# Kernel optimization log

Measured on AMD Instinct MI355X. Metric: run time of the kernel, lower is better.

Reference implementation:

```python
import jax, jax.numpy as jnp
import numpy as np

B, C, N = 8, 256, 2048
H = max(1, C // 8)  # hidden = in_channels // 8 = 32


def setup_inputs() -> dict:
    key = jax.random.key(0)
    ks = jax.random.split(key, 7)
    s = 0.05
    return {
        "x": jax.random.normal(ks[0], (B, C, N), dtype=jnp.float32),
        "wq": jax.random.normal(ks[1], (H, C), dtype=jnp.float32) * s,
        "bq": jax.random.normal(ks[2], (H,), dtype=jnp.float32) * s,
        "wk": jax.random.normal(ks[3], (H, C), dtype=jnp.float32) * s,
        "bk": jax.random.normal(ks[4], (H,), dtype=jnp.float32) * s,
        "wv": jax.random.normal(ks[5], (C, C), dtype=jnp.float32) * s,
        "bv": jax.random.normal(ks[6], (C,), dtype=jnp.float32) * s,
    }


def reference(x, wq, bq, wk, bk, wv, bv):
    # 1x1 Conv1d == per-position linear: weight [out, in]
    q = jnp.einsum('bcn,hc->bnh', x, wq) + bq                  # [B, N, H] (already permuted)
    k = jnp.einsum('bcn,hc->bhn', x, wk) + bk[None, :, None]   # [B, H, N]
    v = jnp.einsum('bcn,dc->bdn', x, wv) + bv[None, :, None]   # [B, C, N]
    energy = jnp.einsum('bnh,bhm->bnm', q, k)                  # [B, N, N] (no scaling, as in source)
    weights = jax.nn.softmax(energy, axis=-1)                  # softmax over last dim
    # out = bmm(value, weights^T): out[b,c,i] = sum_j v[b,c,j] * weights[b,i,j]
    out = jnp.einsum('bcj,bij->bci', v, weights)               # [B, C, N]
    return out + x
```

## Files before the change

kernel.cpp:

```cpp
#include <hip/hip_runtime.h>
#include <hip/hip_bf16.h>
#include <cstdint>
#include <cstddef>

#define B_ 8
#define C_ 256
#define N_ 2048
#define H_ 32
#define VP_ 2064
#define NT_ (N_ / 64)

typedef __bf16 bf8 __attribute__((ext_vector_type(8)));
typedef __bf16 bf4 __attribute__((ext_vector_type(4)));
typedef float f4 __attribute__((ext_vector_type(4)));
typedef float f16v __attribute__((ext_vector_type(16)));

__device__ inline void gload_lds16(const void* g, void* l) {
  __builtin_amdgcn_global_load_lds(
      (const __attribute__((address_space(1))) unsigned int*)g,
      (__attribute__((address_space(3))) unsigned int*)l, 16, 0, 0);
}

__global__ __launch_bounds__(256) void pack_kernel(
    const float* __restrict__ wq, const float* __restrict__ wk,
    const float* __restrict__ wv, const float* __restrict__ bq,
    const float* __restrict__ bk, const float* __restrict__ bv,
    __hip_bfloat16* __restrict__ wpk, float* __restrict__ bpk) {
  const float L2E = 1.44269504088896f;
  int r = blockIdx.x, c = threadIdx.x;
  float v;
  if (r < 256)      v = wv[r * 256 + c];
  else if (r < 288) v = wq[(r - 256) * 256 + c] * L2E;
  else              v = wk[(r - 288) * 256 + c];
  wpk[r * 256 + c] = __float2bfloat16(v);
  if (c == 0) bpk[r] = (r < 256) ? bv[r] : (r < 288 ? bq[r - 256] * L2E : bk[r - 288]);
}

__global__ __launch_bounds__(256) void proj_kernel(
    const float* __restrict__ x, const __hip_bfloat16* __restrict__ wpk,
    const float* __restrict__ bpk, __hip_bfloat16* __restrict__ vbf,
    __hip_bfloat16* __restrict__ qkb) {
  __shared__ __attribute__((aligned(16))) __hip_bfloat16 As[2][320 * 32];
  int tid = threadIdx.x, wv = tid >> 6, lane = tid & 63;
  int b = blockIdx.y;
  int n0 = blockIdx.x * 32;
  int fcol = lane & 15, hi4 = lane >> 4;
  int grow = lane >> 2, gc = (lane & 3) * 8;
  const float* xb = x + (size_t)b * C_ * N_;

#pragma unroll
  for (int g = 0; g < 5; ++g)
    gload_lds16(wpk + (size_t)(wv * 80 + g * 16 + grow) * 256 + gc,
                &As[0][(wv * 80 + g * 16) * 32]);
  float xr[2][8];
#pragma unroll
  for (int j = 0; j < 2; ++j)
#pragma unroll
    for (int e = 0; e < 8; ++e)
      xr[j][e] = xb[(size_t)(hi4 * 8 + e) * N_ + n0 + j * 16 + fcol];

  f4 acc[5][2] = {};
  for (int t = 0; t < 8; ++t) {
    int buf = t & 1;
    __syncthreads();
    if (t < 7) {
      int k1 = (t + 1) * 32;
#pragma unroll
      for (int g = 0; g < 5; ++g)
        gload_lds16(wpk + (size_t)(wv * 80 + g * 16 + grow) * 256 + k1 + gc,
                    &As[buf ^ 1][(wv * 80 + g * 16) * 32]);
    }
    bf8 bfr[2];
#pragma unroll
    for (int j = 0; j < 2; ++j)
#pragma unroll
      for (int e = 0; e < 8; ++e) bfr[j][e] = (__bf16)xr[j][e];
    if (t < 7) {
      int k1 = (t + 1) * 32;
#pragma unroll
      for (int j = 0; j < 2; ++j)
#pragma unroll
        for (int e = 0; e < 8; ++e)
          xr[j][e] = xb[(size_t)(k1 + hi4 * 8 + e) * N_ + n0 + j * 16 + fcol];
    }
#pragma unroll
    for (int s = 0; s < 5; ++s) {
      bf8 af = *(const bf8*)&As[buf][(wv * 80 + s * 16 + fcol) * 32 + hi4 * 8];
      acc[s][0] = __builtin_amdgcn_mfma_f32_16x16x32_bf16(af, bfr[0], acc[s][0], 0, 0, 0);
      acc[s][1] = __builtin_amdgcn_mfma_f32_16x16x32_bf16(af, bfr[1], acc[s][1], 0, 0, 0);
    }
  }
  int rq = hi4 * 4;
#pragma unroll
  for (int s = 0; s < 5; ++s)
#pragma unroll
    for (int r = 0; r < 4; ++r) {
      int m = wv * 80 + s * 16 + rq + r;
      float bias = bpk[m];
#pragma unroll
      for (int j = 0; j < 2; ++j) {
        int n = n0 + j * 16 + fcol;
        float val = acc[s][j][r] + bias;
        if (m < 256)
          vbf[((size_t)b * C_ + m) * VP_ + n] = __float2bfloat16(val);
        else
          qkb[((size_t)b * N_ + n) * 64 + (m - 256)] = __float2bfloat16(val);
      }
    }
}

#define ATTN_BODY(T, BUF, KC0, KC1, KN0, KN1, VC0, VC1, VC2, VC3)              \
  {                                                                            \
    const __hip_bfloat16* pr_ = &pS[BUF][l31][hi * 8];                         \
    bf8 pf0_ = *(const bf8*)(pr_ + 0);                                         \
    bf8 pf4_ = *(const bf8*)(pr_ + 32 * 88);                                   \
    bf8 pf1_ = *(const bf8*)(pr_ + 16);                                        \
    bf8 pf5_ = *(const bf8*)(pr_ + 32 * 88 + 16);                              \
    bf8 pf2_ = *(const bf8*)(pr_ + 32);                                        \
    bf8 pf6_ = *(const bf8*)(pr_ + 32 * 88 + 32);                              \
    bf8 pf3_ = *(const bf8*)(pr_ + 48);                                        \
    bf8 pf7_ = *(const bf8*)(pr_ + 32 * 88 + 48);                              \
    f16v s_ = {};                                                              \
    if ((T) + 1 < NT_) {                                                       \
      s_ = __builtin_amdgcn_mfma_f32_32x32x16_bf16(KC0, qf0, s_, 0, 0, 0);     \
      s_ = __builtin_amdgcn_mfma_f32_32x32x16_bf16(KC1, qf1, s_, 0, 0, 0);     \
    }                                                                          \
    {                                                                          \
      int tn_ = (T) + 2 < NT_ ? (T) + 2 : NT_ - 1;                             \
      const __hip_bfloat16* kpn_ = kp + (size_t)tn_ * 64 * 64;                 \
      KN0 = *(const bf8*)kpn_;                                                 \
      KN1 = *(const bf8*)(kpn_ + 16);                                          \
    }                                                                          \
    __builtin_amdgcn_s_setprio(1);                                             \
    acc0 = __builtin_amdgcn_mfma_f32_32x32x16_bf16(VC0, pf0_, acc0, 0, 0, 0);  \
    acc1 = __builtin_amdgcn_mfma_f32_32x32x16_bf16(VC0, pf4_, acc1, 0, 0, 0);  \
    acc0 = __builtin_amdgcn_mfma_f32_32x32x16_bf16(VC1, pf1_, acc0, 0, 0, 0);  \
    acc1 = __builtin_amdgcn_mfma_f32_32x32x16_bf16(VC1, pf5_, acc1, 0, 0, 0);  \
    acc0 = __builtin_amdgcn_mfma_f32_32x32x16_bf16(VC2, pf2_, acc0, 0, 0, 0);  \
    acc1 = __builtin_amdgcn_mfma_f32_32x32x16_bf16(VC2, pf6_, acc1, 0, 0, 0);  \
    acc0 = __builtin_amdgcn_mfma_f32_32x32x16_bf16(VC3, pf3_, acc0, 0, 0, 0);  \
    acc1 = __builtin_amdgcn_mfma_f32_32x32x16_bf16(VC3, pf7_, acc1, 0, 0, 0);  \
    __builtin_amdgcn_s_setprio(0);                                             \
    {                                                                          \
      int tn_ = (T) + 2 < NT_ ? (T) + 2 : NT_ - 1;                             \
      const __hip_bfloat16* vpn_ = vR + tn_ * 64;                              \
      VC0 = *(const bf8*)vpn_;                                                 \
      VC1 = *(const bf8*)(vpn_ + 16);                                          \
      VC2 = *(const bf8*)(vpn_ + 32);                                          \
      VC3 = *(const bf8*)(vpn_ + 48);                                          \
    }                                                                          \
    if ((T) + 1 < NT_) {                                                       \
      _Pragma("unroll")                                                        \
      for (int r = 0; r < 16; ++r) s_[r] = __builtin_amdgcn_exp2f(s_[r]);      \
      _Pragma("unroll")                                                        \
      for (int r = 0; r < 16; r += 2) { lp0 += s_[r]; lp1 += s_[r + 1]; }      \
      __hip_bfloat16* pw_ = &pS[(BUF) ^ 1][ws_i * 32 + l31][ws_j * 32 + 4 * hi];\
      _Pragma("unroll")                                                        \
      for (int q = 0; q < 4; ++q) {                                            \
        bf4 tb_;                                                               \
        tb_[0] = (__bf16)s_[4 * q + 0];                                        \
        tb_[1] = (__bf16)s_[4 * q + 1];                                        \
        tb_[2] = (__bf16)s_[4 * q + 2];                                        \
        tb_[3] = (__bf16)s_[4 * q + 3];                                        \
        *(bf4*)(pw_ + 8 * q) = tb_;                                            \
      }                                                                        \
      asm volatile("s_waitcnt lgkmcnt(0)" ::: "memory");                       \
      __builtin_amdgcn_sched_barrier(0);                                       \
      __builtin_amdgcn_s_barrier();                                            \
      __builtin_amdgcn_sched_barrier(0);                                       \
    }                                                                          \
  }

__global__ __launch_bounds__(256, 2) void fused_attn(
    const __hip_bfloat16* __restrict__ qk,
    const __hip_bfloat16* __restrict__ vbf,
    const float* __restrict__ x, float* __restrict__ out) {
  __shared__ __attribute__((aligned(16))) __hip_bfloat16 pS[2][64][88];
  __shared__ float lSp[2][64];
  int tid = threadIdx.x;
  int wv = tid >> 6, lane = tid & 63;
  int l31 = lane & 31, hi = lane >> 5;
  int ws_i = wv >> 1, ws_j = wv & 1;
  int blk = blockIdx.x;
  int b = blk & 7;
  int rest = blk >> 3;
  int c0 = (rest & 1) * 128;
  int i0 = (rest >> 1) * 64;

  const __hip_bfloat16* qkB = qk + (size_t)b * N_ * 64;
  const __hip_bfloat16* qp = qkB + (size_t)(i0 + ws_i * 32 + l31) * 64 + hi * 8;
  bf8 qf0 = *(const bf8*)qp;
  bf8 qf1 = *(const bf8*)(qp + 16);
  const __hip_bfloat16* kp = qkB + (size_t)(ws_j * 32 + l31) * 64 + 32 + hi * 8;
  const __hip_bfloat16* vR =
      vbf + ((size_t)b * C_ + c0 + wv * 32 + l31) * VP_ + hi * 8;

  bf8 k00 = *(const bf8*)kp;
  bf8 k01 = *(const bf8*)(kp + 16);
  bf8 kO0 = *(const bf8*)(kp + 64 * 64);
  bf8 kO1 = *(const bf8*)(kp + 64 * 64 + 16);
  bf8 kE0, kE1;
  bf8 vE0 = *(const bf8*)vR;
  bf8 vE1 = *(const bf8*)(vR + 16);
  bf8 vE2 = *(const bf8*)(vR + 32);
  bf8 vE3 = *(const bf8*)(vR + 48);
  bf8 vO0 = *(const bf8*)(vR + 64);
  bf8 vO1 = *(const bf8*)(vR + 64 + 16);
  bf8 vO2 = *(const bf8*)(vR + 64 + 32);
  bf8 vO3 = *(const bf8*)(vR + 64 + 48);

  f16v acc0 = {}, acc1 = {};
  float lp0 = 0.f, lp1 = 0.f;

  {
    f16v s_ = {};
    s_ = __builtin_amdgcn_mfma_f32_32x32x16_bf16(k00, qf0, s_, 0, 0, 0);
    s_ = __builtin_amdgcn_mfma_f32_32x32x16_bf16(k01, qf1, s_, 0, 0, 0);
#pragma unroll
    for (int r = 0; r < 16; ++r) s_[r] = __builtin_amdgcn_exp2f(s_[r]);
#pragma unroll
    for (int r = 0; r < 16; r += 2) { lp0 += s_[r]; lp1 += s_[r + 1]; }
    __hip_bfloat16* pw_ = &pS[0][ws_i * 32 + l31][ws_j * 32 + 4 * hi];
#pragma unroll
    for (int q = 0; q < 4; ++q) {
      bf4 tb_;
      tb_[0] = (__bf16)s_[4 * q + 0];
      tb_[1] = (__bf16)s_[4 * q + 1];
      tb_[2] = (__bf16)s_[4 * q + 2];
      tb_[3] = (__bf16)s_[4 * q + 3];
      *(bf4*)(pw_ + 8 * q) = tb_;
    }
    asm volatile("s_waitcnt lgkmcnt(0)" ::: "memory");
    __builtin_amdgcn_sched_barrier(0);
    __builtin_amdgcn_s_barrier();
    __builtin_amdgcn_sched_barrier(0);
  }

  for (int tt = 0; tt < NT_; tt += 2) {
    ATTN_BODY(tt,     0, kO0, kO1, kE0, kE1, vE0, vE1, vE2, vE3)
    ATTN_BODY(tt + 1, 1, kE0, kE1, kO0, kO1, vO0, vO1, vO2, vO3)
  }
#undef ATTN_BODY

  float lp = lp0 + lp1;
  lp += __shfl_xor(lp, 32);
  if (lane < 32) lSp[ws_j][ws_i * 32 + l31] = lp;
  __syncthreads();
  float linv0 = 1.0f / (lSp[0][l31] + lSp[1][l31]);
  float linv1 = 1.0f / (lSp[0][32 + l31] + lSp[1][32 + l31]);

  const float* xr = x + (size_t)b * C_ * N_;
  float* op = out + (size_t)b * C_ * N_;
#pragma unroll
  for (int r = 0; r < 16; ++r) {
    int crow = (r & 3) + 8 * (r >> 2) + 4 * hi;
    size_t o = (size_t)(c0 + wv * 32 + crow) * N_ + i0 + l31;
    op[o] = acc0[r] * linv0 + xr[o];
    op[o + 32] = acc1[r] * linv1 + xr[o + 32];
  }
}

extern "C" void kernel_launch(void* const* d_in, const int* in_sizes, int n_in,
                              void* d_out, int out_size, void* d_ws, size_t ws_size,
                              hipStream_t stream) {
  const float* x  = (const float*)d_in[0];
  const float* wq = (const float*)d_in[1];
  const float* bq = (const float*)d_in[2];
  const float* wk = (const float*)d_in[3];
  const float* bk = (const float*)d_in[4];
  const float* wv = (const float*)d_in[5];
  const float* bv = (const float*)d_in[6];
  float* out = (float*)d_out;

  char* ws = (char*)d_ws;
  __hip_bfloat16* qkb = (__hip_bfloat16*)ws;
  __hip_bfloat16* vbf = (__hip_bfloat16*)(ws + (2u << 20));
  __hip_bfloat16* wpk = (__hip_bfloat16*)(ws + 10551296u);
  float*          bpk = (float*)(ws + 10551296u + 163840u);

  pack_kernel<<<dim3(320), 256, 0, stream>>>(wq, wk, wv, bq, bk, bv, wpk, bpk);
  proj_kernel<<<dim3(N_ / 32, B_), 256, 0, stream>>>(x, wpk, bpk, vbf, qkb);
  fused_attn<<<dim3(512), 256, 0, stream>>>(qkb, vbf, x, out);
}
```

Measured before the change: 128.2 us.

## Switch attention MFMAs from 32x32x16 to 16x16x32 bf16 tiles

```diff
diff --git a/kernel.cpp b/kernel.cpp
--- a/kernel.cpp
+++ b/kernel.cpp
@@ -13,7 +13,6 @@
 typedef __bf16 bf8 __attribute__((ext_vector_type(8)));
 typedef __bf16 bf4 __attribute__((ext_vector_type(4)));
 typedef float f4 __attribute__((ext_vector_type(4)));
-typedef float f16v __attribute__((ext_vector_type(16)));
 
 __device__ inline void gload_lds16(const void* g, void* l) {
   __builtin_amdgcn_global_load_lds(
@@ -109,60 +108,81 @@
     }
 }
 
-#define ATTN_BODY(T, BUF, KC0, KC1, KN0, KN1, VC0, VC1, VC2, VC3)              \
+#define MFMA16(A, B, C) __builtin_amdgcn_mfma_f32_16x16x32_bf16(A, B, C, 0, 0, 0)
+
+#define ATTN_BODY(T, BUF, KC0, KC1, KN0, KN1, VA, VB, VC, VD)                  \
   {                                                                            \
-    const __hip_bfloat16* pr_ = &pS[BUF][l31][hi * 8];                         \
-    bf8 pf0_ = *(const bf8*)(pr_ + 0);                                         \
-    bf8 pf4_ = *(const bf8*)(pr_ + 32 * 88);                                   \
-    bf8 pf1_ = *(const bf8*)(pr_ + 16);                                        \
-    bf8 pf5_ = *(const bf8*)(pr_ + 32 * 88 + 16);                              \
-    bf8 pf2_ = *(const bf8*)(pr_ + 32);                                        \
-    bf8 pf6_ = *(const bf8*)(pr_ + 32 * 88 + 32);                              \
-    bf8 pf3_ = *(const bf8*)(pr_ + 48);                                        \
-    bf8 pf7_ = *(const bf8*)(pr_ + 32 * 88 + 48);                              \
-    f16v s_ = {};                                                              \
+    bf8 pf00 = *(const bf8*)&pS[BUF][ 0 + li][ 0 + lg8];                       \
+    bf8 pf10 = *(const bf8*)&pS[BUF][16 + li][ 0 + lg8];                       \
+    bf8 pf20 = *(const bf8*)&pS[BUF][32 + li][ 0 + lg8];                       \
+    bf8 pf30 = *(const bf8*)&pS[BUF][48 + li][ 0 + lg8];                       \
+    bf8 pf01 = *(const bf8*)&pS[BUF][ 0 + li][32 + lg8];                       \
+    bf8 pf11 = *(const bf8*)&pS[BUF][16 + li][32 + lg8];                       \
+    bf8 pf21 = *(const bf8*)&pS[BUF][32 + li][32 + lg8];                       \
+    bf8 pf31 = *(const bf8*)&pS[BUF][48 + li][32 + lg8];                       \
+    f4 s00 = {}, s01 = {}, s10 = {}, s11 = {};                                 \
     if ((T) + 1 < NT_) {                                                       \
-      s_ = __builtin_amdgcn_mfma_f32_32x32x16_bf16(KC0, qf0, s_, 0, 0, 0);     \
-      s_ = __builtin_amdgcn_mfma_f32_32x32x16_bf16(KC1, qf1, s_, 0, 0, 0);     \
+      s00 = MFMA16(KC0, qf0, s00);                                             \
+      s01 = MFMA16(KC0, qf1, s01);                                             \
+      s10 = MFMA16(KC1, qf0, s10);                                             \
+      s11 = MFMA16(KC1, qf1, s11);                                             \
     }                                                                          \
     {                                                                          \
       int tn_ = (T) + 2 < NT_ ? (T) + 2 : NT_ - 1;                             \
       const __hip_bfloat16* kpn_ = kp + (size_t)tn_ * 64 * 64;                 \
       KN0 = *(const bf8*)kpn_;                                                 \
-      KN1 = *(const bf8*)(kpn_ + 16);                                          \
+      KN1 = *(const bf8*)(kpn_ + 16 * 64);                                     \
     }                                                                          \
     __builtin_amdgcn_s_setprio(1);                                             \
-    acc0 = __builtin_amdgcn_mfma_f32_32x32x16_bf16(VC0, pf0_, acc0, 0, 0, 0);  \
-    acc1 = __builtin_amdgcn_mfma_f32_32x32x16_bf16(VC0, pf4_, acc1, 0, 0, 0);  \
-    acc0 = __builtin_amdgcn_mfma_f32_32x32x16_bf16(VC1, pf1_, acc0, 0, 0, 0);  \
-    acc1 = __builtin_amdgcn_mfma_f32_32x32x16_bf16(VC1, pf5_, acc1, 0, 0, 0);  \
-    acc0 = __builtin_amdgcn_mfma_f32_32x32x16_bf16(VC2, pf2_, acc0, 0, 0, 0);  \
-    acc1 = __builtin_amdgcn_mfma_f32_32x32x16_bf16(VC2, pf6_, acc1, 0, 0, 0);  \
-    acc0 = __builtin_amdgcn_mfma_f32_32x32x16_bf16(VC3, pf3_, acc0, 0, 0, 0);  \
-    acc1 = __builtin_amdgcn_mfma_f32_32x32x16_bf16(VC3, pf7_, acc1, 0, 0, 0);  \
+    acc[0][0] = MFMA16(VA, pf00, acc[0][0]);                                   \
+    acc[0][1] = MFMA16(VA, pf10, acc[0][1]);                                   \
+    acc[0][2] = MFMA16(VA, pf20, acc[0][2]);                                   \
+    acc[0][3] = MFMA16(VA, pf30, acc[0][3]);                                   \
+    acc[1][0] = MFMA16(VC, pf00, acc[1][0]);                                   \
+    acc[1][1] = MFMA16(VC, pf10, acc[1][1]);                                   \
+    acc[1][2] = MFMA16(VC, pf20, acc[1][2]);                                   \
+    acc[1][3] = MFMA16(VC, pf30, acc[1][3]);                                   \
+    acc[0][0] = MFMA16(VB, pf01, acc[0][0]);                                   \
+    acc[0][1] = MFMA16(VB, pf11, acc[0][1]);                                   \
+    acc[0][2] = MFMA16(VB, pf21, acc[0][2]);                                   \
+    acc[0][3] = MFMA16(VB, pf31, acc[0][3]);                                   \
+    acc[1][0] = MFMA16(VD, pf01, acc[1][0]);                                   \
+    acc[1][1] = MFMA16(VD, pf11, acc[1][1]);                                   \
+    acc[1][2] = MFMA16(VD, pf21, acc[1][2]);                                   \
+    acc[1][3] = MFMA16(VD, pf31, acc[1][3]);                                   \
     __builtin_amdgcn_s_setprio(0);                                             \
     {                                                                          \
       int tn_ = (T) + 2 < NT_ ? (T) + 2 : NT_ - 1;                             \
       const __hip_bfloat16* vpn_ = vR + tn_ * 64;                              \
-      VC0 = *(const bf8*)vpn_;                                                 \
-      VC1 = *(const bf8*)(vpn_ + 16);                                          \
-      VC2 = *(const bf8*)(vpn_ + 32);                                          \
-      VC3 = *(const bf8*)(vpn_ + 48);                                          \
+      VA = *(const bf8*)vpn_;                                                  \
+      VB = *(const bf8*)(vpn_ + 32);                                           \
+      VC = *(const bf8*)(vpn_ + 16 * VP_);                                     \
+      VD = *(const bf8*)(vpn_ + 16 * VP_ + 32);                                \
     }                                                                          \
     if ((T) + 1 < NT_) {                                                       \
       _Pragma("unroll")                                                        \
-      for (int r = 0; r < 16; ++r) s_[r] = __builtin_amdgcn_exp2f(s_[r]);      \
+      for (int m = 0; m < 4; ++m) {                                            \
+        s00[m] = __builtin_amdgcn_exp2f(s00[m]);                               \
+        s01[m] = __builtin_amdgcn_exp2f(s01[m]);                               \
+        s10[m] = __builtin_amdgcn_exp2f(s10[m]);                               \
+        s11[m] = __builtin_amdgcn_exp2f(s11[m]);                               \
+      }                                                                        \
       _Pragma("unroll")                                                        \
-      for (int r = 0; r < 16; r += 2) { lp0 += s_[r]; lp1 += s_[r + 1]; }      \
-      __hip_bfloat16* pw_ = &pS[(BUF) ^ 1][ws_i * 32 + l31][ws_j * 32 + 4 * hi];\
-      _Pragma("unroll")                                                        \
-      for (int q = 0; q < 4; ++q) {                                            \
-        bf4 tb_;                                                               \
-        tb_[0] = (__bf16)s_[4 * q + 0];                                        \
-        tb_[1] = (__bf16)s_[4 * q + 1];                                        \
-        tb_[2] = (__bf16)s_[4 * q + 2];                                        \
-        tb_[3] = (__bf16)s_[4 * q + 3];                                        \
-        *(bf4*)(pw_ + 8 * q) = tb_;                                            \
+      for (int m = 0; m < 4; ++m) {                                            \
+        lp0 += s00[m] + s10[m];                                                \
+        lp1 += s01[m] + s11[m];                                                \
+      }                                                                        \
+      {                                                                        \
+        bf4 t0, t1, t2, t3;                                                    \
+        _Pragma("unroll")                                                      \
+        for (int m = 0; m < 4; ++m) {                                          \
+          t0[m] = (__bf16)s00[m]; t1[m] = (__bf16)s01[m];                      \
+          t2[m] = (__bf16)s10[m]; t3[m] = (__bf16)s11[m];                      \
+        }                                                                      \
+        *(bf4*)&pS[(BUF) ^ 1][ws_i * 32 +  0 + li][ws_j * 32 +  0 + lg4] = t0; \
+        *(bf4*)&pS[(BUF) ^ 1][ws_i * 32 + 16 + li][ws_j * 32 +  0 + lg4] = t1; \
+        *(bf4*)&pS[(BUF) ^ 1][ws_i * 32 +  0 + li][ws_j * 32 + 16 + lg4] = t2; \
+        *(bf4*)&pS[(BUF) ^ 1][ws_i * 32 + 16 + li][ws_j * 32 + 16 + lg4] = t3; \
       }                                                                        \
       asm volatile("s_waitcnt lgkmcnt(0)" ::: "memory");                       \
       __builtin_amdgcn_sched_barrier(0);                                       \
@@ -179,7 +199,8 @@
   __shared__ float lSp[2][64];
   int tid = threadIdx.x;
   int wv = tid >> 6, lane = tid & 63;
-  int l31 = lane & 31, hi = lane >> 5;
+  int li = lane & 15, lg = lane >> 4;
+  int lg8 = lg * 8, lg4 = lg * 4;
   int ws_i = wv >> 1, ws_j = wv & 1;
   int blk = blockIdx.x;
   int b = blk & 7;
@@ -188,48 +209,57 @@
   int i0 = (rest >> 1) * 64;
 
   const __hip_bfloat16* qkB = qk + (size_t)b * N_ * 64;
-  const __hip_bfloat16* qp = qkB + (size_t)(i0 + ws_i * 32 + l31) * 64 + hi * 8;
-  bf8 qf0 = *(const bf8*)qp;
-  bf8 qf1 = *(const bf8*)(qp + 16);
-  const __hip_bfloat16* kp = qkB + (size_t)(ws_j * 32 + l31) * 64 + 32 + hi * 8;
+  bf8 qf0 = *(const bf8*)&qkB[(size_t)(i0 + ws_i * 32 +  0 + li) * 64 + lg8];
+  bf8 qf1 = *(const bf8*)&qkB[(size_t)(i0 + ws_i * 32 + 16 + li) * 64 + lg8];
+  const __hip_bfloat16* kp = qkB + (size_t)(ws_j * 32 + li) * 64 + 32 + lg8;
   const __hip_bfloat16* vR =
-      vbf + ((size_t)b * C_ + c0 + wv * 32 + l31) * VP_ + hi * 8;
+      vbf + ((size_t)b * C_ + c0 + wv * 32 + li) * VP_ + lg8;
 
   bf8 k00 = *(const bf8*)kp;
-  bf8 k01 = *(const bf8*)(kp + 16);
+  bf8 k01 = *(const bf8*)(kp + 16 * 64);
   bf8 kO0 = *(const bf8*)(kp + 64 * 64);
-  bf8 kO1 = *(const bf8*)(kp + 64 * 64 + 16);
+  bf8 kO1 = *(const bf8*)(kp + 64 * 64 + 16 * 64);
   bf8 kE0, kE1;
-  bf8 vE0 = *(const bf8*)vR;
-  bf8 vE1 = *(const bf8*)(vR + 16);
-  bf8 vE2 = *(const bf8*)(vR + 32);
-  bf8 vE3 = *(const bf8*)(vR + 48);
-  bf8 vO0 = *(const bf8*)(vR + 64);
-  bf8 vO1 = *(const bf8*)(vR + 64 + 16);
-  bf8 vO2 = *(const bf8*)(vR + 64 + 32);
-  bf8 vO3 = *(const bf8*)(vR + 64 + 48);
-
-  f16v acc0 = {}, acc1 = {};
+  bf8 vEA = *(const bf8*)vR;
+  bf8 vEB = *(const bf8*)(vR + 32);
+  bf8 vEC = *(const bf8*)(vR + 16 * VP_);
+  bf8 vED = *(const bf8*)(vR + 16 * VP_ + 32);
+  bf8 vOA = *(const bf8*)(vR + 64);
+  bf8 vOB = *(const bf8*)(vR + 64 + 32);
+  bf8 vOC = *(const bf8*)(vR + 16 * VP_ + 64);
+  bf8 vOD = *(const bf8*)(vR + 16 * VP_ + 64 + 32);
+
+  f4 acc[2][4] = {};
   float lp0 = 0.f, lp1 = 0.f;
 
   {
-    f16v s_ = {};
-    s_ = __builtin_amdgcn_mfma_f32_32x32x16_bf16(k00, qf0, s_, 0, 0, 0);
-    s_ = __builtin_amdgcn_mfma_f32_32x32x16_bf16(k01, qf1, s_, 0, 0, 0);
-#pragma unroll
-    for (int r = 0; r < 16; ++r) s_[r] = __builtin_amdgcn_exp2f(s_[r]);
-#pragma unroll
-    for (int r = 0; r < 16; r += 2) { lp0 += s_[r]; lp1 += s_[r + 1]; }
-    __hip_bfloat16* pw_ = &pS[0][ws_i * 32 + l31][ws_j * 32 + 4 * hi];
-#pragma unroll
-    for (int q = 0; q < 4; ++q) {
-      bf4 tb_;
-      tb_[0] = (__bf16)s_[4 * q + 0];
-      tb_[1] = (__bf16)s_[4 * q + 1];
-      tb_[2] = (__bf16)s_[4 * q + 2];
-      tb_[3] = (__bf16)s_[4 * q + 3];
-      *(bf4*)(pw_ + 8 * q) = tb_;
-    }
+    f4 s00 = {}, s01 = {}, s10 = {}, s11 = {};
+    s00 = MFMA16(k00, qf0, s00);
+    s01 = MFMA16(k00, qf1, s01);
+    s10 = MFMA16(k01, qf0, s10);
+    s11 = MFMA16(k01, qf1, s11);
+#pragma unroll
+    for (int m = 0; m < 4; ++m) {
+      s00[m] = __builtin_amdgcn_exp2f(s00[m]);
+      s01[m] = __builtin_amdgcn_exp2f(s01[m]);
+      s10[m] = __builtin_amdgcn_exp2f(s10[m]);
+      s11[m] = __builtin_amdgcn_exp2f(s11[m]);
+    }
+#pragma unroll
+    for (int m = 0; m < 4; ++m) {
+      lp0 += s00[m] + s10[m];
+      lp1 += s01[m] + s11[m];
+    }
+    bf4 t0, t1, t2, t3;
+#pragma unroll
+    for (int m = 0; m < 4; ++m) {
+      t0[m] = (__bf16)s00[m]; t1[m] = (__bf16)s01[m];
+      t2[m] = (__bf16)s10[m]; t3[m] = (__bf16)s11[m];
+    }
+    *(bf4*)&pS[0][ws_i * 32 +  0 + li][ws_j * 32 +  0 + lg4] = t0;
+    *(bf4*)&pS[0][ws_i * 32 + 16 + li][ws_j * 32 +  0 + lg4] = t1;
+    *(bf4*)&pS[0][ws_i * 32 +  0 + li][ws_j * 32 + 16 + lg4] = t2;
+    *(bf4*)&pS[0][ws_i * 32 + 16 + li][ws_j * 32 + 16 + lg4] = t3;
     asm volatile("s_waitcnt lgkmcnt(0)" ::: "memory");
     __builtin_amdgcn_sched_barrier(0);
     __builtin_amdgcn_s_barrier();
@@ -237,27 +267,34 @@
   }
 
   for (int tt = 0; tt < NT_; tt += 2) {
-    ATTN_BODY(tt,     0, kO0, kO1, kE0, kE1, vE0, vE1, vE2, vE3)
-    ATTN_BODY(tt + 1, 1, kE0, kE1, kO0, kO1, vO0, vO1, vO2, vO3)
+    ATTN_BODY(tt,     0, kO0, kO1, kE0, kE1, vEA, vEB, vEC, vED)
+    ATTN_BODY(tt + 1, 1, kE0, kE1, kO0, kO1, vOA, vOB, vOC, vOD)
   }
 #undef ATTN_BODY
 
-  float lp = lp0 + lp1;
-  lp += __shfl_xor(lp, 32);
-  if (lane < 32) lSp[ws_j][ws_i * 32 + l31] = lp;
+  lp0 += __shfl_xor(lp0, 16); lp0 += __shfl_xor(lp0, 32);
+  lp1 += __shfl_xor(lp1, 16); lp1 += __shfl_xor(lp1, 32);
+  if (lane < 16)      lSp[ws_j][ws_i * 32 + lane] = lp0;
+  else if (lane < 32) lSp[ws_j][ws_i * 32 + 16 + (lane & 15)] = lp1;
   __syncthreads();
-  float linv0 = 1.0f / (lSp[0][l31] + lSp[1][l31]);
-  float linv1 = 1.0f / (lSp[0][32 + l31] + lSp[1][32 + l31]);
+  float linv0 = 1.0f / (lSp[0][ 0 + li] + lSp[1][ 0 + li]);
+  float linv1 = 1.0f / (lSp[0][16 + li] + lSp[1][16 + li]);
+  float linv2 = 1.0f / (lSp[0][32 + li] + lSp[1][32 + li]);
+  float linv3 = 1.0f / (lSp[0][48 + li] + lSp[1][48 + li]);
 
   const float* xr = x + (size_t)b * C_ * N_;
   float* op = out + (size_t)b * C_ * N_;
 #pragma unroll
-  for (int r = 0; r < 16; ++r) {
-    int crow = (r & 3) + 8 * (r >> 2) + 4 * hi;
-    size_t o = (size_t)(c0 + wv * 32 + crow) * N_ + i0 + l31;
-    op[o] = acc0[r] * linv0 + xr[o];
-    op[o + 32] = acc1[r] * linv1 + xr[o + 32];
-  }
+  for (int cs = 0; cs < 2; ++cs)
+#pragma unroll
+    for (int m = 0; m < 4; ++m) {
+      int c = c0 + wv * 32 + cs * 16 + lg4 + m;
+      size_t base = (size_t)c * N_ + i0;
+      op[base +  0 + li] = acc[cs][0][m] * linv0 + xr[base +  0 + li];
+      op[base + 16 + li] = acc[cs][1][m] * linv1 + xr[base + 16 + li];
+      op[base + 32 + li] = acc[cs][2][m] * linv2 + xr[base + 32 + li];
+      op[base + 48 + li] = acc[cs][3][m] * linv3 + xr[base + 48 + li];
+    }
 }
 
 extern "C" void kernel_launch(void* const* d_in, const int* in_sizes, int n_in,
```

After: 129.3 us. No clear change (+0.8%).
